# Kernel tuning notes

Hardware: AMD Instinct MI355X
Metric: run time of the kernel (lower is better)

Reference implementation:

```python
import jax, jax.numpy as jnp
import numpy as np

B, SQ, SK, DK, DV = 16, 2048, 2048, 64, 64


def setup_inputs() -> dict:
    key = jax.random.key(0)
    kq, kk, kv, km = jax.random.split(key, 4)
    Q = jax.random.normal(kq, (B, SQ, DK), dtype=jnp.float32)
    K = jax.random.normal(kk, (B, SK, DK), dtype=jnp.float32)
    V = jax.random.normal(kv, (B, SK, DV), dtype=jnp.float32)
    mask = jax.random.randint(km, (B, 1, SK), 0, 2, dtype=jnp.int32)
    return {"Q": Q, "K": K, "V": V, "mask": mask}


def reference(Q, K, V, mask):
    d = K.shape[-1]
    # scores: (B, SQ, SK) -- full attention matrix, as in the torch module
    attn = jnp.einsum("bqd,bkd->bqk", Q, K) / (d ** 0.5)
    masked = mask == 0  # (B, 1, SK), broadcasts over query dim
    attn = jnp.where(masked, jnp.float32(-1e9), attn)
    attn = jax.nn.softmax(attn, axis=-1)
    attn = jnp.where(masked, jnp.float32(0.0), attn)
    output = jnp.einsum("bqk,bkv->bqv", attn, V)
    return (output, attn)
```

## Files before the change

kernel.cpp:

```cpp
#include <hip/hip_runtime.h>
#include <hip/hip_bf16.h>

#define NB   16
#define SQL  2048
#define SKL  2048
#define DKL  64
#define DVL  64
#define NE   (NB * SQL * DKL)

typedef __attribute__((ext_vector_type(8))) short short8;
typedef __attribute__((ext_vector_type(4))) short s16x4;
typedef __attribute__((ext_vector_type(4))) float f32x4;

#define VST 56
#define PST 56

#define SCALE_LOG2E 0.1803368801111204f
#define EXP2F(x) __builtin_amdgcn_exp2f(x)

__device__ __forceinline__ short f2bf(float x) {
    unsigned u = __builtin_bit_cast(unsigned, x);
    u = (u + 0x7fffu + ((u >> 16) & 1u)) >> 16;
    return (short)u;
}
__device__ __forceinline__ float bf2f(short s) {
    return __builtin_bit_cast(float, ((unsigned)(unsigned short)s) << 16);
}

__global__ __launch_bounds__(256)
void prep(const float* __restrict__ Q, const float* __restrict__ K,
          const float* __restrict__ V, short* __restrict__ ws)
{
    short* qhi = ws;
    short* qlo = ws + (size_t)NE;
    short* khi = ws + (size_t)2 * NE;
    short* klo = ws + (size_t)3 * NE;
    short* vb  = ws + (size_t)4 * NE;

    size_t i4 = ((size_t)blockIdx.x * 256 + threadIdx.x) * 4;
    if (i4 >= NE) return;

    f32x4 q = *(const f32x4*)(Q + i4);
    f32x4 k = *(const f32x4*)(K + i4);
    f32x4 v = *(const f32x4*)(V + i4);
    s16x4 qh, ql, kh, kl, vv;
    #pragma unroll
    for (int j = 0; j < 4; j++) {
        qh[j] = f2bf(q[j]);  ql[j] = f2bf(q[j] - bf2f(qh[j]));
        kh[j] = f2bf(k[j]);  kl[j] = f2bf(k[j] - bf2f(kh[j]));
        vv[j] = f2bf(v[j]);
    }
    *(s16x4*)(qhi + i4) = qh;
    *(s16x4*)(qlo + i4) = ql;
    *(s16x4*)(khi + i4) = kh;
    *(s16x4*)(klo + i4) = kl;
    *(s16x4*)(vb  + i4) = vv;
}

__device__ __forceinline__ void qk_tiles(const short* __restrict__ khi,
                                         const short* __restrict__ klo, int kb,
                                         int l15, int quad,
                                         short8 qa0h, short8 qa1h,
                                         short8 qa0l, short8 qa1l,
                                         f32x4& s0, f32x4& s1) {
    size_t o0 = (size_t)(kb + l15) * DKL + quad * 8;
    size_t o1 = (size_t)(kb + 16 + l15) * DKL + quad * 8;
    short8 h0l = *(const short8*)(khi + o0);
    short8 h0h = *(const short8*)(khi + o0 + 32);
    short8 h1l = *(const short8*)(khi + o1);
    short8 h1h = *(const short8*)(khi + o1 + 32);
    short8 l0l = *(const short8*)(klo + o0);
    short8 l0h = *(const short8*)(klo + o0 + 32);
    short8 l1l = *(const short8*)(klo + o1);
    short8 l1h = *(const short8*)(klo + o1 + 32);
    f32x4 z = {0.f, 0.f, 0.f, 0.f};
    s0 = __builtin_amdgcn_mfma_f32_16x16x32_bf16(qa0h, h0l, z, 0, 0, 0);
    s0 = __builtin_amdgcn_mfma_f32_16x16x32_bf16(qa1h, h0h, s0, 0, 0, 0);
    s0 = __builtin_amdgcn_mfma_f32_16x16x32_bf16(qa0h, l0l, s0, 0, 0, 0);
    s0 = __builtin_amdgcn_mfma_f32_16x16x32_bf16(qa1h, l0h, s0, 0, 0, 0);
    s0 = __builtin_amdgcn_mfma_f32_16x16x32_bf16(qa0l, h0l, s0, 0, 0, 0);
    s0 = __builtin_amdgcn_mfma_f32_16x16x32_bf16(qa1l, h0h, s0, 0, 0, 0);
    s1 = __builtin_amdgcn_mfma_f32_16x16x32_bf16(qa0h, h1l, z, 0, 0, 0);
    s1 = __builtin_amdgcn_mfma_f32_16x16x32_bf16(qa1h, h1h, s1, 0, 0, 0);
    s1 = __builtin_amdgcn_mfma_f32_16x16x32_bf16(qa0h, l1l, s1, 0, 0, 0);
    s1 = __builtin_amdgcn_mfma_f32_16x16x32_bf16(qa1h, l1h, s1, 0, 0, 0);
    s1 = __builtin_amdgcn_mfma_f32_16x16x32_bf16(qa0l, h1l, s1, 0, 0, 0);
    s1 = __builtin_amdgcn_mfma_f32_16x16x32_bf16(qa1l, h1h, s1, 0, 0, 0);
}

__global__ __launch_bounds__(256)
void attn_fwd(const short* __restrict__ ws, const int* __restrict__ mask,
              float* __restrict__ out, float* __restrict__ attn)
{
    __shared__ float s_bias[SKL];
    __shared__ short s_vt[64 * VST];
    __shared__ short s_p[4 * 16 * PST];

    const int tid  = threadIdx.x;
    const int wave = tid >> 6;
    const int l15  = tid & 15;
    const int quad = (tid & 63) >> 4;

    const int b     = blockIdx.x >> 5;
    const int qblk  = blockIdx.x & 31;
    const int qbase = qblk * 64 + wave * 16;

    for (int i = tid; i < SKL; i += 256)
        s_bias[i] = mask[b * SKL + i] ? 0.0f : -1e9f;
    __syncthreads();

    const short* qhi = ws +             (size_t)(b * SQL + qbase) * DKL;
    const short* qlo = ws + (size_t)NE + (size_t)(b * SQL + qbase) * DKL;
    const short* khi = ws + (size_t)2 * NE + (size_t)b * SKL * DKL;
    const short* klo = ws + (size_t)3 * NE + (size_t)b * SKL * DKL;
    const short* vb  = ws + (size_t)4 * NE + (size_t)b * SKL * DVL;

    short8 qa0h = *(const short8*)(qhi + (size_t)l15 * DKL + quad * 8);
    short8 qa1h = *(const short8*)(qhi + (size_t)l15 * DKL + 32 + quad * 8);
    short8 qa0l = *(const short8*)(qlo + (size_t)l15 * DKL + quad * 8);
    short8 qa1l = *(const short8*)(qlo + (size_t)l15 * DKL + 32 + quad * 8);

    float lsum[4] = {0.f, 0.f, 0.f, 0.f};
    for (int kb = 0; kb < SKL; kb += 32) {
        f32x4 s0, s1;
        qk_tiles(khi, klo, kb, l15, quad, qa0h, qa1h, qa0l, qa1l, s0, s1);
        float bias0 = s_bias[kb + l15];
        float bias1 = s_bias[kb + 16 + l15];
        #pragma unroll
        for (int r = 0; r < 4; r++) {
            lsum[r] += EXP2F(fmaf(s0[r], SCALE_LOG2E, bias0));
            lsum[r] += EXP2F(fmaf(s1[r], SCALE_LOG2E, bias1));
        }
    }
    #pragma unroll
    for (int off = 1; off <= 8; off <<= 1) {
        #pragma unroll
        for (int r = 0; r < 4; r++)
            lsum[r] += __shfl_xor(lsum[r], off, 64);
    }
    float inv_l[4];
    #pragma unroll
    for (int r = 0; r < 4; r++) inv_l[r] = 1.0f / lsum[r];

    f32x4 acc[4];
    #pragma unroll
    for (int vt = 0; vt < 4; vt++) { f32x4 z = {0.f,0.f,0.f,0.f}; acc[vt] = z; }

    const int vk  = tid & 31;
    const int vv0 = (tid >> 5) * 8;
    short* pw = s_p + wave * 16 * PST;

    for (int kb = 0; kb < SKL; kb += 32) {
        __syncthreads();
        {
            short8 vvv = *(const short8*)(vb + (size_t)(kb + vk) * DVL + vv0);
            #pragma unroll
            for (int j = 0; j < 8; j++)
                s_vt[(vv0 + j) * VST + vk] = vvv[j];
        }
        __syncthreads();

        f32x4 s0, s1;
        qk_tiles(khi, klo, kb, l15, quad, qa0h, qa1h, qa0l, qa1l, s0, s1);
        float bias0 = s_bias[kb + l15];
        float bias1 = s_bias[kb + 16 + l15];

        const size_t arow = (size_t)(b * SQL + qbase + quad * 4) * SKL + kb;
        #pragma unroll
        for (int r = 0; r < 4; r++) {
            float p0 = EXP2F(fmaf(s0[r], SCALE_LOG2E, bias0)) * inv_l[r];
            float p1 = EXP2F(fmaf(s1[r], SCALE_LOG2E, bias1)) * inv_l[r];
            attn[arow + (size_t)r * SKL + l15]      = p0;
            attn[arow + (size_t)r * SKL + 16 + l15] = p1;
            pw[(quad * 4 + r) * PST + l15]      = f2bf(p0);
            pw[(quad * 4 + r) * PST + 16 + l15] = f2bf(p1);
        }

        short8 pa = *(const short8*)(pw + l15 * PST + quad * 8);
        #pragma unroll
        for (int vt = 0; vt < 4; vt++) {
            short8 bvv = *(const short8*)(s_vt + (vt * 16 + l15) * VST + quad * 8);
            acc[vt] = __builtin_amdgcn_mfma_f32_16x16x32_bf16(pa, bvv, acc[vt], 0, 0, 0);
        }
    }

    #pragma unroll
    for (int vt = 0; vt < 4; vt++) {
        #pragma unroll
        for (int r = 0; r < 4; r++)
            out[(size_t)(b * SQL + qbase + quad * 4 + r) * DVL + vt * 16 + l15] =
                acc[vt][r];
    }
}

extern "C" void kernel_launch(void* const* d_in, const int* in_sizes, int n_in,
                              void* d_out, int out_size, void* d_ws, size_t ws_size,
                              hipStream_t stream) {
    const float* Q    = (const float*)d_in[0];
    const float* K    = (const float*)d_in[1];
    const float* V    = (const float*)d_in[2];
    const int*   mask = (const int*)d_in[3];
    float* out  = (float*)d_out;
    float* attn = out + (size_t)NB * SQL * DVL;
    short* ws   = (short*)d_ws;

    prep<<<dim3(NE / (256 * 4)), dim3(256), 0, stream>>>(Q, K, V, ws);
    attn_fwd<<<dim3(NB * (SQL / 64)), dim3(256), 0, stream>>>(ws, mask, out, attn);
}
```

Measured before the change: 526.0 us.

## Split key range across waves, pre-transpose V globally, drop per-tile block syncs

The attention kernel now gives each block 32 query rows and splits the key range in half across wave pairs. Partial row sums and output accumulators are combined through shared memory, which doubles the number of blocks. V is transposed into bf16 by a separate kernel, so the PV MFMA reads B operands straight from global memory. This removes the per-tile shared-memory transpose and its two __syncthreads. The mask bias is read directly from global memory instead of a shared table, and the QK hi/lo products are split into two independent accumulation chains. The cost is an extra kernel launch, strided global loads of V, and the cross-wave reductions.

```diff
diff --git a/kernel.cpp b/kernel.cpp
--- a/kernel.cpp
+++ b/kernel.cpp
@@ -12,7 +12,6 @@
 typedef __attribute__((ext_vector_type(4))) short s16x4;
 typedef __attribute__((ext_vector_type(4))) float f32x4;
 
-#define VST 56
 #define PST 56
 
 #define SCALE_LOG2E 0.1803368801111204f
@@ -29,32 +28,48 @@
 
 __global__ __launch_bounds__(256)
 void prep(const float* __restrict__ Q, const float* __restrict__ K,
-          const float* __restrict__ V, short* __restrict__ ws)
+          short* __restrict__ ws)
 {
     short* qhi = ws;
     short* qlo = ws + (size_t)NE;
     short* khi = ws + (size_t)2 * NE;
     short* klo = ws + (size_t)3 * NE;
-    short* vb  = ws + (size_t)4 * NE;
 
     size_t i4 = ((size_t)blockIdx.x * 256 + threadIdx.x) * 4;
     if (i4 >= NE) return;
 
     f32x4 q = *(const f32x4*)(Q + i4);
     f32x4 k = *(const f32x4*)(K + i4);
-    f32x4 v = *(const f32x4*)(V + i4);
-    s16x4 qh, ql, kh, kl, vv;
+    s16x4 qh, ql, kh, kl;
     #pragma unroll
     for (int j = 0; j < 4; j++) {
         qh[j] = f2bf(q[j]);  ql[j] = f2bf(q[j] - bf2f(qh[j]));
         kh[j] = f2bf(k[j]);  kl[j] = f2bf(k[j] - bf2f(kh[j]));
-        vv[j] = f2bf(v[j]);
     }
     *(s16x4*)(qhi + i4) = qh;
     *(s16x4*)(qlo + i4) = ql;
     *(s16x4*)(khi + i4) = kh;
     *(s16x4*)(klo + i4) = kl;
-    *(s16x4*)(vb  + i4) = vv;
+}
+
+__global__ __launch_bounds__(256)
+void vtrans(const float* __restrict__ V, short* __restrict__ vt)
+{
+    const int b  = blockIdx.x >> 5;
+    const int kt = blockIdx.x & 31;
+    const int v  = threadIdx.x & 63;
+    const int kg = (threadIdx.x >> 6) * 16;
+
+    const float* src = V + ((size_t)b * SKL + kt * 64 + kg) * DVL + v;
+    short* dst = vt + (size_t)b * DVL * SKL + (size_t)v * SKL + kt * 64 + kg;
+
+    short8 lo8, hi8;
+    #pragma unroll
+    for (int j = 0; j < 8; j++) lo8[j] = f2bf(src[(size_t)j * DVL]);
+    #pragma unroll
+    for (int j = 0; j < 8; j++) hi8[j] = f2bf(src[(size_t)(j + 8) * DVL]);
+    *(short8*)dst = lo8;
+    *(short8*)(dst + 8) = hi8;
 }
 
 __device__ __forceinline__ void qk_tiles(const short* __restrict__ khi,
@@ -64,7 +79,7 @@
                                          short8 qa0l, short8 qa1l,
                                          f32x4& s0, f32x4& s1) {
     size_t o0 = (size_t)(kb + l15) * DKL + quad * 8;
-    size_t o1 = (size_t)(kb + 16 + l15) * DKL + quad * 8;
+    size_t o1 = o0 + (size_t)16 * DKL;
     short8 h0l = *(const short8*)(khi + o0);
     short8 h0h = *(const short8*)(khi + o0 + 32);
     short8 h1l = *(const short8*)(khi + o1);
@@ -74,46 +89,47 @@
     short8 l1l = *(const short8*)(klo + o1);
     short8 l1h = *(const short8*)(klo + o1 + 32);
     f32x4 z = {0.f, 0.f, 0.f, 0.f};
-    s0 = __builtin_amdgcn_mfma_f32_16x16x32_bf16(qa0h, h0l, z, 0, 0, 0);
-    s0 = __builtin_amdgcn_mfma_f32_16x16x32_bf16(qa1h, h0h, s0, 0, 0, 0);
-    s0 = __builtin_amdgcn_mfma_f32_16x16x32_bf16(qa0h, l0l, s0, 0, 0, 0);
-    s0 = __builtin_amdgcn_mfma_f32_16x16x32_bf16(qa1h, l0h, s0, 0, 0, 0);
-    s0 = __builtin_amdgcn_mfma_f32_16x16x32_bf16(qa0l, h0l, s0, 0, 0, 0);
-    s0 = __builtin_amdgcn_mfma_f32_16x16x32_bf16(qa1l, h0h, s0, 0, 0, 0);
-    s1 = __builtin_amdgcn_mfma_f32_16x16x32_bf16(qa0h, h1l, z, 0, 0, 0);
-    s1 = __builtin_amdgcn_mfma_f32_16x16x32_bf16(qa1h, h1h, s1, 0, 0, 0);
-    s1 = __builtin_amdgcn_mfma_f32_16x16x32_bf16(qa0h, l1l, s1, 0, 0, 0);
-    s1 = __builtin_amdgcn_mfma_f32_16x16x32_bf16(qa1h, l1h, s1, 0, 0, 0);
-    s1 = __builtin_amdgcn_mfma_f32_16x16x32_bf16(qa0l, h1l, s1, 0, 0, 0);
-    s1 = __builtin_amdgcn_mfma_f32_16x16x32_bf16(qa1l, h1h, s1, 0, 0, 0);
-}
-
-__global__ __launch_bounds__(256)
+    f32x4 a0 = __builtin_amdgcn_mfma_f32_16x16x32_bf16(qa0h, h0l, z, 0, 0, 0);
+    a0 = __builtin_amdgcn_mfma_f32_16x16x32_bf16(qa1h, h0h, a0, 0, 0, 0);
+    f32x4 b0 = __builtin_amdgcn_mfma_f32_16x16x32_bf16(qa0l, h0l, z, 0, 0, 0);
+    b0 = __builtin_amdgcn_mfma_f32_16x16x32_bf16(qa1l, h0h, b0, 0, 0, 0);
+    b0 = __builtin_amdgcn_mfma_f32_16x16x32_bf16(qa0h, l0l, b0, 0, 0, 0);
+    b0 = __builtin_amdgcn_mfma_f32_16x16x32_bf16(qa1h, l0h, b0, 0, 0, 0);
+    f32x4 a1 = __builtin_amdgcn_mfma_f32_16x16x32_bf16(qa0h, h1l, z, 0, 0, 0);
+    a1 = __builtin_amdgcn_mfma_f32_16x16x32_bf16(qa1h, h1h, a1, 0, 0, 0);
+    f32x4 b1 = __builtin_amdgcn_mfma_f32_16x16x32_bf16(qa0l, h1l, z, 0, 0, 0);
+    b1 = __builtin_amdgcn_mfma_f32_16x16x32_bf16(qa1l, h1h, b1, 0, 0, 0);
+    b1 = __builtin_amdgcn_mfma_f32_16x16x32_bf16(qa0h, l1l, b1, 0, 0, 0);
+    b1 = __builtin_amdgcn_mfma_f32_16x16x32_bf16(qa1h, l1h, b1, 0, 0, 0);
+    s0 = a0 + b0;
+    s1 = a1 + b1;
+}
+
+__global__ __launch_bounds__(256, 4)
 void attn_fwd(const short* __restrict__ ws, const int* __restrict__ mask,
               float* __restrict__ out, float* __restrict__ attn)
 {
-    __shared__ float s_bias[SKL];
-    __shared__ short s_vt[64 * VST];
+    __shared__ float s_l[2][16][2];
+    __shared__ float s_o[2][16][64];
     __shared__ short s_p[4 * 16 * PST];
 
     const int tid  = threadIdx.x;
     const int wave = tid >> 6;
     const int l15  = tid & 15;
     const int quad = (tid & 63) >> 4;
-
-    const int b     = blockIdx.x >> 5;
-    const int qblk  = blockIdx.x & 31;
-    const int qbase = qblk * 64 + wave * 16;
-
-    for (int i = tid; i < SKL; i += 256)
-        s_bias[i] = mask[b * SKL + i] ? 0.0f : -1e9f;
-    __syncthreads();
-
-    const short* qhi = ws +             (size_t)(b * SQL + qbase) * DKL;
-    const short* qlo = ws + (size_t)NE + (size_t)(b * SQL + qbase) * DKL;
-    const short* khi = ws + (size_t)2 * NE + (size_t)b * SKL * DKL;
-    const short* klo = ws + (size_t)3 * NE + (size_t)b * SKL * DKL;
-    const short* vb  = ws + (size_t)4 * NE + (size_t)b * SKL * DVL;
+    const int qt   = wave & 1;
+    const int kh   = wave >> 1;
+
+    const int b  = blockIdx.x >> 6;
+    const int qb = (blockIdx.x & 63) * 32 + qt * 16;
+    const int k0 = kh * (SKL / 2);
+
+    const short* qhi  = ws + (size_t)(b * SQL + qb) * DKL;
+    const short* qlo  = qhi + (size_t)NE;
+    const short* khiB = ws + (size_t)2 * NE + (size_t)b * SKL * DKL;
+    const short* kloB = khiB + (size_t)NE;
+    const short* vtB  = ws + (size_t)4 * NE + (size_t)b * DVL * SKL;
+    const int*  maskB = mask + b * SKL;
 
     short8 qa0h = *(const short8*)(qhi + (size_t)l15 * DKL + quad * 8);
     short8 qa1h = *(const short8*)(qhi + (size_t)l15 * DKL + 32 + quad * 8);
@@ -121,11 +137,12 @@
     short8 qa1l = *(const short8*)(qlo + (size_t)l15 * DKL + 32 + quad * 8);
 
     float lsum[4] = {0.f, 0.f, 0.f, 0.f};
-    for (int kb = 0; kb < SKL; kb += 32) {
+    #pragma unroll 2
+    for (int kb = k0; kb < k0 + SKL / 2; kb += 32) {
         f32x4 s0, s1;
-        qk_tiles(khi, klo, kb, l15, quad, qa0h, qa1h, qa0l, qa1l, s0, s1);
-        float bias0 = s_bias[kb + l15];
-        float bias1 = s_bias[kb + 16 + l15];
+        qk_tiles(khiB, kloB, kb, l15, quad, qa0h, qa1h, qa0l, qa1l, s0, s1);
+        float bias0 = maskB[kb + l15]      ? 0.0f : -1e9f;
+        float bias1 = maskB[kb + 16 + l15] ? 0.0f : -1e9f;
         #pragma unroll
         for (int r = 0; r < 4; r++) {
             lsum[r] += EXP2F(fmaf(s0[r], SCALE_LOG2E, bias0));
@@ -138,34 +155,30 @@
         for (int r = 0; r < 4; r++)
             lsum[r] += __shfl_xor(lsum[r], off, 64);
     }
+    if (l15 == 0) {
+        #pragma unroll
+        for (int r = 0; r < 4; r++)
+            s_l[qt][quad * 4 + r][kh] = lsum[r];
+    }
+    __syncthreads();
     float inv_l[4];
     #pragma unroll
-    for (int r = 0; r < 4; r++) inv_l[r] = 1.0f / lsum[r];
+    for (int r = 0; r < 4; r++)
+        inv_l[r] = 1.0f / (s_l[qt][quad * 4 + r][0] + s_l[qt][quad * 4 + r][1]);
 
     f32x4 acc[4];
     #pragma unroll
     for (int vt = 0; vt < 4; vt++) { f32x4 z = {0.f,0.f,0.f,0.f}; acc[vt] = z; }
 
-    const int vk  = tid & 31;
-    const int vv0 = (tid >> 5) * 8;
     short* pw = s_p + wave * 16 * PST;
 
-    for (int kb = 0; kb < SKL; kb += 32) {
-        __syncthreads();
-        {
-            short8 vvv = *(const short8*)(vb + (size_t)(kb + vk) * DVL + vv0);
-            #pragma unroll
-            for (int j = 0; j < 8; j++)
-                s_vt[(vv0 + j) * VST + vk] = vvv[j];
-        }
-        __syncthreads();
-
+    for (int kb = k0; kb < k0 + SKL / 2; kb += 32) {
         f32x4 s0, s1;
-        qk_tiles(khi, klo, kb, l15, quad, qa0h, qa1h, qa0l, qa1l, s0, s1);
-        float bias0 = s_bias[kb + l15];
-        float bias1 = s_bias[kb + 16 + l15];
-
-        const size_t arow = (size_t)(b * SQL + qbase + quad * 4) * SKL + kb;
+        qk_tiles(khiB, kloB, kb, l15, quad, qa0h, qa1h, qa0l, qa1l, s0, s1);
+        float bias0 = maskB[kb + l15]      ? 0.0f : -1e9f;
+        float bias1 = maskB[kb + 16 + l15] ? 0.0f : -1e9f;
+
+        const size_t arow = (size_t)(b * SQL + qb + quad * 4) * SKL + kb;
         #pragma unroll
         for (int r = 0; r < 4; r++) {
             float p0 = EXP2F(fmaf(s0[r], SCALE_LOG2E, bias0)) * inv_l[r];
@@ -179,17 +192,26 @@
         short8 pa = *(const short8*)(pw + l15 * PST + quad * 8);
         #pragma unroll
         for (int vt = 0; vt < 4; vt++) {
-            short8 bvv = *(const short8*)(s_vt + (vt * 16 + l15) * VST + quad * 8);
+            short8 bvv = *(const short8*)(vtB + (size_t)(vt * 16 + l15) * SKL + kb + quad * 8);
             acc[vt] = __builtin_amdgcn_mfma_f32_16x16x32_bf16(pa, bvv, acc[vt], 0, 0, 0);
         }
     }
 
-    #pragma unroll
-    for (int vt = 0; vt < 4; vt++) {
-        #pragma unroll
-        for (int r = 0; r < 4; r++)
-            out[(size_t)(b * SQL + qbase + quad * 4 + r) * DVL + vt * 16 + l15] =
-                acc[vt][r];
+    if (kh == 1) {
+        #pragma unroll
+        for (int vt = 0; vt < 4; vt++)
+            #pragma unroll
+            for (int r = 0; r < 4; r++)
+                s_o[qt][quad * 4 + r][vt * 16 + l15] = acc[vt][r];
+    }
+    __syncthreads();
+    if (kh == 0) {
+        #pragma unroll
+        for (int vt = 0; vt < 4; vt++)
+            #pragma unroll
+            for (int r = 0; r < 4; r++)
+                out[(size_t)(b * SQL + qb + quad * 4 + r) * DVL + vt * 16 + l15] =
+                    acc[vt][r] + s_o[qt][quad * 4 + r][vt * 16 + l15];
     }
 }
 
@@ -204,6 +226,7 @@
     float* attn = out + (size_t)NB * SQL * DVL;
     short* ws   = (short*)d_ws;
 
-    prep<<<dim3(NE / (256 * 4)), dim3(256), 0, stream>>>(Q, K, V, ws);
-    attn_fwd<<<dim3(NB * (SQL / 64)), dim3(256), 0, stream>>>(ws, mask, out, attn);
-}
+    prep<<<dim3(NE / (256 * 4)), dim3(256), 0, stream>>>(Q, K, ws);
+    vtrans<<<dim3(NB * (SKL / 64)), dim3(256), 0, stream>>>(V, ws + (size_t)4 * NE);
+    attn_fwd<<<dim3(NB * (SQL / 32)), dim3(256), 0, stream>>>(ws, mask, out, attn);
+}
```

Result: slower. 551.9 us (+4.9%).
